# Kernel optimization log

Hardware: AMD Instinct MI355X
Metric: run time of the kernel (lower is better)

The kernel has to match this reference:

```python
import jax, jax.numpy as jnp
import numpy as np

B, T, I, H = 128, 2048, 256, 256


def setup_inputs() -> dict:
    key = jax.random.key(0)
    k1, k2, k3 = jax.random.split(key, 3)
    # xavier-uniform-like scale for weights
    s_x = float(np.sqrt(6.0 / (I + H)))
    s_h = float(np.sqrt(6.0 / (H + H)))
    return {
        "x": jax.random.normal(k1, (B, T, I), dtype=jnp.float32),
        "w_x": jax.random.uniform(k2, (I, H), jnp.float32, -s_x, s_x),
        "b_x": jnp.zeros((H,), jnp.float32),
        "w_h": jax.random.uniform(k3, (H, H), jnp.float32, -s_h, s_h),
        "b_h": jnp.zeros((H,), jnp.float32),
    }


def reference(x, w_x, b_x, w_h, b_h):
    # The original computes identical pre-activations for all four gates:
    # z = x_t @ w_x + b_x + h @ w_h + b_h; f=i=o=sigmoid(z), g=tanh(z).
    # Precompute the input projection for all timesteps in one GEMM.
    b, t, _ = x.shape
    h0 = jnp.zeros((b, w_h.shape[0]), x.dtype)
    c0 = jnp.zeros_like(h0)
    xproj = jnp.einsum('bti,ih->tbh', x, w_x) + b_x  # [T, B, H]

    def step(carry, xp_t):
        h, c = carry
        z = xp_t + h @ w_h + b_h
        s = jax.nn.sigmoid(z)   # f_t == i_t == o_t
        g = jnp.tanh(z)         # g_t
        c_new = s * c + s * g
        h_new = s * jnp.tanh(c_new)
        return (h_new, c_new), None

    (h_t, c_t), _ = jax.lax.scan(step, (h0, c0), xproj)
    return (h_t, c_t)
```

## Files before the change

### kernel.cpp

```cpp
#include <hip/hip_runtime.h>
#include <stdint.h>

#define B_ 128
#define T_ 2048
#define I_ 256
#define H_ 256


__device__ __forceinline__ void gates_sg(float z, float& s, float& g){
  float az = fabsf(z);
  float a  = __expf(-az);
  float r1 = __builtin_amdgcn_rcpf(1.0f + a);
  s = (z >= 0.0f) ? r1 : a * r1;
  float a2 = a * a;
  float gm = (1.0f - a2) * __builtin_amdgcn_rcpf(1.0f + a2);
  g = (z >= 0.0f) ? gm : -gm;
}
__device__ __forceinline__ float tanh_stable(float c){
  float ac = fabsf(c);
  float u  = __expf(-2.0f * ac);
  float tm = (1.0f - u) * __builtin_amdgcn_rcpf(1.0f + u);
  return (c >= 0.0f) ? tm : -tm;
}

__device__ __forceinline__ float bcast_lane(float v, int srclane){
  return __builtin_bit_cast(float,
      __builtin_amdgcn_readlane(__builtin_bit_cast(int, v), srclane));
}

#define FMA4(hs, wv, ax, ay, az, aw)            \
  ax = fmaf(hs, wv.x, ax); ay = fmaf(hs, wv.y, ay); \
  az = fmaf(hs, wv.z, az); aw = fmaf(hs, wv.w, aw);

#define PIN4(v) asm volatile("" : "+v"(v.x), "+v"(v.y), "+v"(v.z), "+v"(v.w))


__global__ __launch_bounds__(512, 2) void xproj_k(
    const float* __restrict__ x, const float* __restrict__ w_x,
    const float* __restrict__ b_x, const float* __restrict__ b_h,
    float* __restrict__ xp, int t0c, int Tc)
{
  const int tid  = threadIdx.x;
  const int wv   = tid >> 6;
  const int lane = tid & 63;
  const int ks   = wv * 32;

  float4 w4[32];
  #pragma unroll
  for (int kk = 0; kk < 32; ++kk)
    w4[kk] = *(const float4*)&w_x[(ks + kk) * H_ + 4 * lane];

  float bias = 0.0f;
  if (tid < 256) bias = b_x[tid] + b_h[tid];

  __shared__ float4 xs4[256];
  __shared__ float  pb[8][4][256];

  const int rows_per_b = Tc >> 2;
  const int nblk  = (B_ * Tc) >> 2;
  const int iters = (nblk + gridDim.x - 1) / gridDim.x;
  const int bid0  = blockIdx.x * iters;

  float4 r = make_float4(0,0,0,0);
  if (tid < 256 && bid0 < nblk){
    const int b  = bid0 / rows_per_b;
    const int t4 = (bid0 - b * rows_per_b) << 2;
    r = ((const float4*)x)[ (int64_t)(b * T_ + t0c + t4) * 64 + tid ];
  }

  for (int i = 0; i < iters; ++i){
    const int bid = bid0 + i;
    const bool valid = bid < nblk;
    if (tid < 256 && valid) xs4[tid] = r;
    __syncthreads();
    if (tid < 256 && bid + 1 < nblk){
      const int bn = bid + 1;
      const int b  = bn / rows_per_b;
      const int t4 = (bn - b * rows_per_b) << 2;
      r = ((const float4*)x)[ (int64_t)(b * T_ + t0c + t4) * 64 + tid ];
    }
    if (valid){
      #pragma unroll
      for (int rr = 0; rr < 4; ++rr){
        const float4* xr = &xs4[rr * 64 + (ks >> 2)];
        float ax = 0.f, ay = 0.f, az = 0.f, aw = 0.f;
        #pragma unroll
        for (int q = 0; q < 8; ++q){
          float4 hv = xr[q];
          FMA4(hv.x, w4[4*q+0], ax, ay, az, aw);
          FMA4(hv.y, w4[4*q+1], ax, ay, az, aw);
          FMA4(hv.z, w4[4*q+2], ax, ay, az, aw);
          FMA4(hv.w, w4[4*q+3], ax, ay, az, aw);
        }
        *(float4*)&pb[wv][rr][4*lane] = make_float4(ax, ay, az, aw);
      }
    }
    __syncthreads();
    if (valid && tid < 256){
      const int b  = bid / rows_per_b;
      const int t4 = (bid - b * rows_per_b) << 2;
      float z0 = bias, z1 = bias, z2 = bias, z3 = bias;
      #pragma unroll
      for (int w = 0; w < 8; ++w){
        z0 += pb[w][0][tid]; z1 += pb[w][1][tid];
        z2 += pb[w][2][tid]; z3 += pb[w][3][tid];
      }
      *(float4*)&xp[ ((int64_t)b * H_ + tid) * Tc + t4 ] = make_float4(z0, z1, z2, z3);
    }
  }
}


__global__ __launch_bounds__(512, 2) void rec_k(
    const float* __restrict__ xp, const float* __restrict__ w_h,
    float* __restrict__ out, int Tc, int init)
{
  const int tid  = threadIdx.x;
  const int wv   = tid >> 6;
  const int lane = tid & 63;
  const int ks   = wv * 32;
  const int b    = blockIdx.x;

  float4 w4[32];
  #pragma unroll
  for (int kk = 0; kk < 32; ++kk)
    w4[kk] = *(const float4*)&w_h[(ks + kk) * H_ + 4 * lane];
  #pragma unroll
  for (int kk = 0; kk < 32; ++kk) PIN4(w4[kk]);

  __shared__ float pbuf[2][8][H_];

  const int  c32   = lane & 31;
  const int  col   = ks + c32;
  const int  hset  = lane >> 5;
  const bool owner = (lane < 32);

  float c = 0.f, hcur = 0.f;
  const float* xpr = xp + ((int64_t)b * H_ + col) * Tc;
  float xarr[4] = {0,0,0,0};
  float4 xq_next = make_float4(0,0,0,0);
  if (owner){
    hcur = init ? 0.f : out[(int64_t)b * H_ + col];
    c    = init ? 0.f : out[(int64_t)B_ * H_ + (int64_t)b * H_ + col];
    xq_next = *(const float4*)xpr;
  }
  int pp = 0;
  for (int t = 0; t < Tc; t += 4){
    if (owner){
      xarr[0] = xq_next.x; xarr[1] = xq_next.y;
      xarr[2] = xq_next.z; xarr[3] = xq_next.w;
      if (t + 4 < Tc) xq_next = *(const float4*)(xpr + t + 4);
    }
    #pragma unroll
    for (int tt = 0; tt < 4; ++tt){
      float ax = 0.f, ay = 0.f, az = 0.f, aw = 0.f;
      #pragma unroll
      for (int q = 0; q < 8; ++q){
        float h0 = bcast_lane(hcur, 4*q+0);
        float h1 = bcast_lane(hcur, 4*q+1);
        float h2 = bcast_lane(hcur, 4*q+2);
        float h3 = bcast_lane(hcur, 4*q+3);
        FMA4(h0, w4[4*q+0], ax, ay, az, aw);
        FMA4(h1, w4[4*q+1], ax, ay, az, aw);
        FMA4(h2, w4[4*q+2], ax, ay, az, aw);
        FMA4(h3, w4[4*q+3], ax, ay, az, aw);
      }
      *(float4*)&pbuf[pp][wv][4*lane] = make_float4(ax, ay, az, aw);
      __syncthreads();
      float sum = pbuf[pp][4*hset+0][col] + pbuf[pp][4*hset+1][col]
                + pbuf[pp][4*hset+2][col] + pbuf[pp][4*hset+3][col];
      sum += __shfl_down(sum, 32, 64);
      if (owner){
        float z = xarr[tt] + sum;
        float s, g; gates_sg(z, s, g);
        c    = s * (c + g);
        hcur = s * tanh_stable(c);
      }
      pp ^= 1;
    }
  }
  if (owner){
    out[(int64_t)b * H_ + col] = hcur;
    out[(int64_t)B_ * H_ + (int64_t)b * H_ + col] = c;
  }
}


__global__ __launch_bounds__(512, 2) void lstm_fused_k(
    const float* __restrict__ x, const float* __restrict__ w_x,
    const float* __restrict__ b_x, const float* __restrict__ w_h,
    const float* __restrict__ b_h, float* __restrict__ out)
{
  const int tid  = threadIdx.x;
  const int wv   = tid >> 6;
  const int lane = tid & 63;
  const int ks   = wv * 32;
  const int b    = blockIdx.x;

  float4 wh4[32], wx4[32];
  #pragma unroll
  for (int kk = 0; kk < 32; ++kk){
    wh4[kk] = *(const float4*)&w_h[(ks + kk) * H_ + 4 * lane];
    wx4[kk] = *(const float4*)&w_x[(ks + kk) * H_ + 4 * lane];
  }
  float bias = 0.0f;
  if (tid < 256) bias = b_x[tid] + b_h[tid];

  __shared__ float hb[2][H_];
  __shared__ float4 xs4[2][64];
  __shared__ float pbuf[8][H_];
  const float* xrow = x + (int64_t)b * T_ * I_;
  if (tid < 256) hb[0][tid] = 0.f;
  if (tid < 64)  xs4[0][tid] = ((const float4*)xrow)[tid];
  __syncthreads();
  float c = 0.f, hn = 0.f;
  int p = 0;
  for (int t = 0; t < T_; ++t){
    const float4* hr = (const float4*)&hb[p][ks];
    const float4* xr = &xs4[p][ks >> 2];
    float ax = 0.f, ay = 0.f, az = 0.f, aw = 0.f;
    #pragma unroll
    for (int q = 0; q < 8; ++q){
      float4 hv = hr[q];
      FMA4(hv.x, wh4[4*q+0], ax, ay, az, aw);
      FMA4(hv.y, wh4[4*q+1], ax, ay, az, aw);
      FMA4(hv.z, wh4[4*q+2], ax, ay, az, aw);
      FMA4(hv.w, wh4[4*q+3], ax, ay, az, aw);
    }
    #pragma unroll
    for (int q = 0; q < 8; ++q){
      float4 xv = xr[q];
      FMA4(xv.x, wx4[4*q+0], ax, ay, az, aw);
      FMA4(xv.y, wx4[4*q+1], ax, ay, az, aw);
      FMA4(xv.z, wx4[4*q+2], ax, ay, az, aw);
      FMA4(xv.w, wx4[4*q+3], ax, ay, az, aw);
    }
    *(float4*)&pbuf[wv][4*lane] = make_float4(ax, ay, az, aw);
    __syncthreads();
    if (tid < 256){
      float z = bias
              + ((pbuf[0][tid] + pbuf[1][tid]) + (pbuf[2][tid] + pbuf[3][tid]))
              + ((pbuf[4][tid] + pbuf[5][tid]) + (pbuf[6][tid] + pbuf[7][tid]));
      float s, g; gates_sg(z, s, g);
      c  = s * (c + g);
      hn = s * tanh_stable(c);
      hb[p ^ 1][tid] = hn;
    } else if (tid < 320 && t + 1 < T_){
      xs4[p ^ 1][tid - 256] = ((const float4*)(xrow + (int64_t)(t + 1) * I_))[tid - 256];
    }
    __syncthreads();
    p ^= 1;
  }
  if (tid < 256){
    out[(int64_t)b * H_ + tid] = hn;
    out[(int64_t)B_ * H_ + (int64_t)b * H_ + tid] = c;
  }
}


extern "C" void kernel_launch(void* const* d_in, const int* in_sizes, int n_in,
                              void* d_out, int out_size, void* d_ws, size_t ws_size,
                              hipStream_t stream)
{
  const float* x   = (const float*)d_in[0];
  const float* w_x = (const float*)d_in[1];
  const float* b_x = (const float*)d_in[2];
  const float* w_h = (const float*)d_in[3];
  const float* b_h = (const float*)d_in[4];
  float* out = (float*)d_out;

  const size_t per_t = (size_t)B_ * H_ * sizeof(float);
  int Tc_max = (int)((ws_size / per_t) & ~(size_t)3);
  if (Tc_max >= 4){
    if (Tc_max > T_) Tc_max = T_;
    int done = 0, first = 1;
    while (done < T_){
      int Tc = (T_ - done < Tc_max) ? (T_ - done) : Tc_max;
      xproj_k<<<512, 512, 0, stream>>>(x, w_x, b_x, b_h, (float*)d_ws, done, Tc);
      rec_k<<<128, 512, 0, stream>>>((const float*)d_ws, w_h, out, Tc, first);
      done += Tc; first = 0;
    }
  } else {
    lstm_fused_k<<<128, 512, 0, stream>>>(x, w_x, b_x, w_h, b_h, out);
  }
}
```

Before: 2.265 ms.

## Split recurrent matvec across 16 waves with quad-replicated gate evaluation

Result: slower. 2.389 ms (+5.5%).

```diff
diff --git a/kernel.cpp b/kernel.cpp
--- a/kernel.cpp
+++ b/kernel.cpp
@@ -26,6 +26,12 @@
 __device__ __forceinline__ float bcast_lane(float v, int srclane){
   return __builtin_bit_cast(float,
       __builtin_amdgcn_readlane(__builtin_bit_cast(int, v), srclane));
+}
+
+template<int CTRL>
+__device__ __forceinline__ float dpp_qperm(float v){
+  return __builtin_bit_cast(float,
+      __builtin_amdgcn_update_dpp(0, __builtin_bit_cast(int, v), CTRL, 0xF, 0xF, true));
 }
 
 #define FMA4(hs, wv, ax, ay, az, aw)            \
@@ -111,75 +117,62 @@
 }
 
 
-__global__ __launch_bounds__(512, 2) void rec_k(
+__global__ __launch_bounds__(1024, 4) void rec_k(
     const float* __restrict__ xp, const float* __restrict__ w_h,
     float* __restrict__ out, int Tc, int init)
 {
-  const int tid  = threadIdx.x;
-  const int wv   = tid >> 6;
-  const int lane = tid & 63;
-  const int ks   = wv * 32;
-  const int b    = blockIdx.x;
-
-  float4 w4[32];
-  #pragma unroll
-  for (int kk = 0; kk < 32; ++kk)
-    w4[kk] = *(const float4*)&w_h[(ks + kk) * H_ + 4 * lane];
-  #pragma unroll
-  for (int kk = 0; kk < 32; ++kk) PIN4(w4[kk]);
-
-  __shared__ float pbuf[2][8][H_];
-
-  const int  c32   = lane & 31;
-  const int  col   = ks + c32;
-  const int  hset  = lane >> 5;
-  const bool owner = (lane < 32);
+  const int tid = threadIdx.x;
+  const int w   = tid >> 6;
+  const int l   = tid & 63;
+  const int g   = l & 3;
+  const int cq  = l >> 2;
+  const int col = w * 16 + cq;
+  const int b   = blockIdx.x;
+
+  float4 wreg[16];
+  #pragma unroll
+  for (int kk = 0; kk < 16; ++kk)
+    wreg[kk] = *(const float4*)&w_h[(16 * w + kk) * H_ + 4 * l];
+  #pragma unroll
+  for (int kk = 0; kk < 16; ++kk) PIN4(wreg[kk]);
+
+  __shared__ float pbuf[2][16][260];
 
   float c = 0.f, hcur = 0.f;
+  if (!init){
+    hcur = out[(int64_t)b * H_ + col];
+    c    = out[(int64_t)B_ * H_ + (int64_t)b * H_ + col];
+  }
+
   const float* xpr = xp + ((int64_t)b * H_ + col) * Tc;
-  float xarr[4] = {0,0,0,0};
-  float4 xq_next = make_float4(0,0,0,0);
-  if (owner){
-    hcur = init ? 0.f : out[(int64_t)b * H_ + col];
-    c    = init ? 0.f : out[(int64_t)B_ * H_ + (int64_t)b * H_ + col];
-    xq_next = *(const float4*)xpr;
-  }
+  float4 xq = *(const float4*)xpr;
+
   int pp = 0;
   for (int t = 0; t < Tc; t += 4){
-    if (owner){
-      xarr[0] = xq_next.x; xarr[1] = xq_next.y;
-      xarr[2] = xq_next.z; xarr[3] = xq_next.w;
-      if (t + 4 < Tc) xq_next = *(const float4*)(xpr + t + 4);
-    }
+    float xa[4] = {xq.x, xq.y, xq.z, xq.w};
+    if (t + 4 < Tc) xq = *(const float4*)(xpr + t + 4);
     #pragma unroll
     for (int tt = 0; tt < 4; ++tt){
       float ax = 0.f, ay = 0.f, az = 0.f, aw = 0.f;
       #pragma unroll
-      for (int q = 0; q < 8; ++q){
-        float h0 = bcast_lane(hcur, 4*q+0);
-        float h1 = bcast_lane(hcur, 4*q+1);
-        float h2 = bcast_lane(hcur, 4*q+2);
-        float h3 = bcast_lane(hcur, 4*q+3);
-        FMA4(h0, w4[4*q+0], ax, ay, az, aw);
-        FMA4(h1, w4[4*q+1], ax, ay, az, aw);
-        FMA4(h2, w4[4*q+2], ax, ay, az, aw);
-        FMA4(h3, w4[4*q+3], ax, ay, az, aw);
+      for (int kk = 0; kk < 16; ++kk){
+        float hk = bcast_lane(hcur, 4 * kk);
+        FMA4(hk, wreg[kk], ax, ay, az, aw);
       }
-      *(float4*)&pbuf[pp][wv][4*lane] = make_float4(ax, ay, az, aw);
+      *(float4*)&pbuf[pp][w][4 * l] = make_float4(ax, ay, az, aw);
       __syncthreads();
-      float sum = pbuf[pp][4*hset+0][col] + pbuf[pp][4*hset+1][col]
-                + pbuf[pp][4*hset+2][col] + pbuf[pp][4*hset+3][col];
-      sum += __shfl_down(sum, 32, 64);
-      if (owner){
-        float z = xarr[tt] + sum;
-        float s, g; gates_sg(z, s, g);
-        c    = s * (c + g);
-        hcur = s * tanh_stable(c);
-      }
+      float sum = (pbuf[pp][4*g+0][col] + pbuf[pp][4*g+1][col])
+                + (pbuf[pp][4*g+2][col] + pbuf[pp][4*g+3][col]);
+      sum += dpp_qperm<0xB1>(sum);
+      sum += dpp_qperm<0x4E>(sum);
+      float z = xa[tt] + sum;
+      float s, gg; gates_sg(z, s, gg);
+      c    = s * (c + gg);
+      hcur = s * tanh_stable(c);
       pp ^= 1;
     }
   }
-  if (owner){
+  if (g == 0){
     out[(int64_t)b * H_ + col] = hcur;
     out[(int64_t)B_ * H_ + (int64_t)b * H_ + col] = c;
   }
@@ -277,7 +270,7 @@
     while (done < T_){
       int Tc = (T_ - done < Tc_max) ? (T_ - done) : Tc_max;
       xproj_k<<<512, 512, 0, stream>>>(x, w_x, b_x, b_h, (float*)d_ws, done, Tc);
-      rec_k<<<128, 512, 0, stream>>>((const float*)d_ws, w_h, out, Tc, first);
+      rec_k<<<128, 1024, 0, stream>>>((const float*)d_ws, w_h, out, Tc, first);
       done += Tc; first = 0;
     }
   } else {
```
